# Optimization experiments

Hardware: AMD Instinct MI355X
Metric: run time of the kernel (lower is better)

The kernel has to match this reference:

```python
import jax, jax.numpy as jnp
import numpy as np

B, S, K = 4, 2048, 8
N_NEURONS, N_BASIS, RANK = 64, 32, 8
D_MODEL, D_HID = 256, 1024


def setup_inputs() -> dict:
    key = jax.random.key(0)
    ks = jax.random.split(key, 10)
    x = jax.random.normal(ks[0], (B, S, D_MODEL), dtype=jnp.float32)
    neuron_idx = jax.random.randint(ks[1], (B, S, K), 0, N_NEURONS)
    w = jax.random.uniform(ks[2], (B, S, K), dtype=jnp.float32)
    neuron_weights = w / jnp.sum(w, axis=-1, keepdims=True)  # softmax-like routing weights
    neuron_recipes = jax.random.normal(ks[3], (N_NEURONS, N_BASIS), dtype=jnp.float32) * 0.5
    sc = 0.1
    basis_A1 = jax.random.normal(ks[4], (N_BASIS, 16, RANK, 8), dtype=jnp.float32) * sc
    basis_A2 = jax.random.normal(ks[5], (N_BASIS, RANK, 16, 8), dtype=jnp.float32) * sc
    basis_B1 = jax.random.normal(ks[6], (N_BASIS, 8, RANK, 32), dtype=jnp.float32) * sc
    basis_B2 = jax.random.normal(ks[7], (N_BASIS, RANK, 8, 32), dtype=jnp.float32) * sc
    w_down_w = jax.random.normal(ks[8], (D_HID, D_MODEL), dtype=jnp.float32) * (1.0 / np.sqrt(D_HID))
    w_down_b = jnp.zeros((D_MODEL,), dtype=jnp.float32)
    return {
        "x": x, "neuron_idx": neuron_idx, "neuron_weights": neuron_weights,
        "neuron_recipes": neuron_recipes,
        "basis_A1": basis_A1, "basis_A2": basis_A2,
        "basis_B1": basis_B1, "basis_B2": basis_B2,
        "w_down_w": w_down_w, "w_down_b": w_down_b,
    }


def reference(x, neuron_idx, neuron_weights, neuron_recipes,
              basis_A1, basis_A2, basis_B1, basis_B2, w_down_w, w_down_b):
    Bt, St, D = x.shape
    # --- routing: gather recipes of selected neurons, softmax, weighted-combine ---
    sel = neuron_recipes[neuron_idx]                       # [B,S,k,n_basis]
    sel = jax.nn.softmax(sel, axis=-1)
    wr = jnp.einsum('bskn,bsk->bsn', sel, neuron_weights)  # [B,S,n_basis]
    # --- build per-token TT cores from basis banks (get_neuron_tt_cores) ---
    cA1 = jnp.einsum('bsn,nirk->bsirk', wr, basis_A1)      # [B,S,16,r,8]
    cA2 = jnp.einsum('bsn,nrjl->bsrjl', wr, basis_A2)      # [B,S,r,16,8]
    cB1 = jnp.einsum('bsn,nirk->bsirk', wr, basis_B1)      # [B,S,8,r,32]
    cB2 = jnp.einsum('bsn,nrjl->bsrjl', wr, basis_B2)      # [B,S,r,8,32]
    # --- TT FFN: 256 -> 64 ---
    x_fold = x.reshape(Bt, St, 16, 16)
    temp = jnp.einsum('bsij,bsirk->bsjrk', x_fold, cA1)
    h = jnp.einsum('bsjrk,bsrjl->bskl', temp, cA2).reshape(Bt, St, 64)
    # --- TT FFN: 64 -> 1024 ---
    h_fold = h.reshape(Bt, St, 8, 8)
    temp = jnp.einsum('bsij,bsirk->bsjrk', h_fold, cB1)
    out = jnp.einsum('bsjrk,bsrjl->bskl', temp, cB2).reshape(Bt, St, D_HID)
    out = jax.nn.gelu(out, approximate=False)              # torch F.gelu default = exact erf
    return out @ w_down_w + w_down_b                       # [B,S,256]
```

## Files before the change

kernel.cpp:

```cpp
#include <hip/hip_runtime.h>
#include <math.h>


typedef unsigned short u16;
typedef __attribute__((ext_vector_type(8))) __bf16 bf16x8;
typedef __attribute__((ext_vector_type(4))) float f32x4;
union ABCast { float4 f; bf16x8 v; };
union BFBits { __bf16 b; u16 u; };
union Pack8 { u16 u[8]; float4 f; };

__device__ __forceinline__ float gelu_exact(float v) {
    return 0.5f * v * (1.0f + erff(v * 0.70710678118654752440f));
}
__device__ __forceinline__ u16 f2bf_bits(float f) { BFBits c; c.b = (__bf16)f; return c.u; }
__device__ __forceinline__ float bfbits2f(u16 u) { BFBits c; c.u = u; return (float)c.b; }

__global__ __launch_bounds__(64) void k_route(
    const int* __restrict__ nidx, const float* __restrict__ nw,
    const float* __restrict__ recipes, float* __restrict__ wr_out,
    u16* __restrict__ wrAh, u16* __restrict__ wrAl)
{
    const int t = blockIdx.x * 64 + threadIdx.x;
    float acc[32];
#pragma unroll
    for (int n = 0; n < 32; n++) acc[n] = 0.f;
#pragma unroll
    for (int k = 0; k < 8; k++) {
        const int   id = nidx[t * 8 + k];
        const float wk = nw[t * 8 + k];
        const float4* row = (const float4*)(recipes + id * 32);
        float v[32];
#pragma unroll
        for (int q = 0; q < 8; q++) {
            float4 f = row[q];
            v[q*4+0] = f.x; v[q*4+1] = f.y; v[q*4+2] = f.z; v[q*4+3] = f.w;
        }
        float m = v[0];
#pragma unroll
        for (int n = 1; n < 32; n++) m = fmaxf(m, v[n]);
        float s = 0.f;
#pragma unroll
        for (int n = 0; n < 32; n++) { float e = expf(v[n] - m); v[n] = e; s += e; }
        const float iv = wk / s;
#pragma unroll
        for (int n = 0; n < 32; n++) acc[n] += v[n] * iv;
    }
    float4* o = (float4*)(wr_out + t * 32);
#pragma unroll
    for (int q = 0; q < 8; q++)
        o[q] = make_float4(acc[q*4+0], acc[q*4+1], acc[q*4+2], acc[q*4+3]);

    const int tg16 = t >> 4, tl = t & 15;
#pragma unroll
    for (int c = 0; c < 4; c++) {
        Pack8 ph, pl;
#pragma unroll
        for (int e = 0; e < 8; e++) {
            const float v = acc[c*8 + e];
            const u16 hb = f2bf_bits(v);
            ph.u[e] = hb;
            pl.u[e] = f2bf_bits(v - bfbits2f(hb));
        }
        const int lane = c * 16 + tl;
        *(float4*)(wrAh + (tg16*64 + lane)*8) = ph.f;
        *(float4*)(wrAl + (tg16*64 + lane)*8) = pl.f;
    }
}

__global__ __launch_bounds__(512) void k_stageA(
    const float* __restrict__ x, const float* __restrict__ wr,
    const float* __restrict__ A1, const float* __restrict__ A2,
    float* __restrict__ h_out)
{
    __shared__ float ca[8 * 1024];
    __shared__ float tl[8 * 1088];
    const int tid = threadIdx.x;
    const int t0  = blockIdx.x * 8;
    {
        const int e2 = tid * 2;
        float2 c[8];
#pragma unroll
        for (int tt = 0; tt < 8; tt++) c[tt] = make_float2(0.f, 0.f);
#pragma unroll 4
        for (int n = 0; n < 32; n++) {
            const float2 a = *(const float2*)(A1 + n * 1024 + e2);
#pragma unroll
            for (int tt = 0; tt < 8; tt++) {
                const float s = wr[(t0 + tt) * 32 + n];
                c[tt].x += s * a.x; c[tt].y += s * a.y;
            }
        }
#pragma unroll
        for (int tt = 0; tt < 8; tt++) *(float2*)(ca + tt * 1024 + e2) = c[tt];
    }
    __syncthreads();
    {
        const int t = tid >> 6, g = tid & 63, j = g >> 2, eh = g & 3;
        float xr[16];
#pragma unroll
        for (int i = 0; i < 16; i++) xr[i] = x[(t0 + t) * 256 + i * 16 + j];
        float tr[16];
#pragma unroll
        for (int q = 0; q < 16; q++) tr[q] = 0.f;
#pragma unroll
        for (int i = 0; i < 16; i++) {
            const float xv = xr[i];
#pragma unroll
            for (int q = 0; q < 4; q++) {
                const float4 cv = *(const float4*)(ca + t * 1024 + i * 64 + eh * 16 + q * 4);
                tr[q*4+0] += xv * cv.x; tr[q*4+1] += xv * cv.y;
                tr[q*4+2] += xv * cv.z; tr[q*4+3] += xv * cv.w;
            }
        }
#pragma unroll
        for (int q = 0; q < 4; q++)
            *(float4*)(tl + t * 1088 + j * 68 + eh * 16 + q * 4) =
                make_float4(tr[q*4+0], tr[q*4+1], tr[q*4+2], tr[q*4+3]);
    }
    __syncthreads();
    {
        const int e2 = tid * 2;
        float2 c[8];
#pragma unroll
        for (int tt = 0; tt < 8; tt++) c[tt] = make_float2(0.f, 0.f);
#pragma unroll 4
        for (int n = 0; n < 32; n++) {
            const float2 a = *(const float2*)(A2 + n * 1024 + e2);
#pragma unroll
            for (int tt = 0; tt < 8; tt++) {
                const float s = wr[(t0 + tt) * 32 + n];
                c[tt].x += s * a.x; c[tt].y += s * a.y;
            }
        }
#pragma unroll
        for (int tt = 0; tt < 8; tt++) *(float2*)(ca + tt * 1024 + e2) = c[tt];
    }
    __syncthreads();
    {
        const int t = tid >> 6, g = tid & 63, k = g >> 3, l = g & 7;
        float acc = 0.f;
#pragma unroll
        for (int j = 0; j < 16; j++) {
#pragma unroll
            for (int r = 0; r < 8; r++) {
                acc += tl[t * 1088 + j * 68 + r * 8 + k] *
                       ca[t * 1024 + r * 128 + j * 8 + l];
            }
        }
        h_out[(t0 + t) * 64 + g] = acc;
    }
}

__global__ __launch_bounds__(256) void k_bsplit(
    const float* __restrict__ B1, const float* __restrict__ B2,
    u16* __restrict__ o1h, u16* __restrict__ o1l,
    u16* __restrict__ o2h, u16* __restrict__ o2l)
{
    const int slot = blockIdx.x * 256 + threadIdx.x;
    const int bank = slot >> 13, r = (slot >> 10) & 7, g = (slot >> 6) & 15, l = slot & 63;
    const int c = l & 15, nb = 8 * (l >> 4);
    const int base = (bank == 0)
        ? ((g >> 1) * 256 + r * 32 + (g & 1) * 16 + c)
        : (r * 256 + (g >> 1) * 32 + (g & 1) * 16 + c);
    const float* S = (bank ? B2 : B1) + base + nb * 2048;
    Pack8 ph, pl;
#pragma unroll
    for (int e = 0; e < 8; e++) {
        const float v = S[e * 2048];
        const u16 hb = f2bf_bits(v);
        ph.u[e] = hb;
        pl.u[e] = f2bf_bits(v - bfbits2f(hb));
    }
    const int d = ((r * 16 + g) * 64 + l) * 8;
    *(float4*)((bank ? o2h : o1h) + d) = ph.f;
    *(float4*)((bank ? o2l : o1l) + d) = pl.f;
}

__global__ __launch_bounds__(256) void k_wsplit(
    const float* __restrict__ W, u16* __restrict__ wfh, u16* __restrict__ wfl)
{
    const int slot = blockIdx.x * 256 + threadIdx.x;
    const int ng = slot >> 11, kc = (slot >> 6) & 31, l = slot & 63;
    const float* S = W + (kc * 32 + 8 * (l >> 4)) * 256 + ng * 16 + (l & 15);
    Pack8 ph, pl;
#pragma unroll
    for (int e = 0; e < 8; e++) {
        const float v = S[e * 256];
        const u16 hb = f2bf_bits(v);
        ph.u[e] = hb;
        pl.u[e] = f2bf_bits(v - bfbits2f(hb));
    }
    const int d = ((ng * 32 + kc) * 64 + l) * 8;
    *(float4*)(wfh + d) = ph.f;
    *(float4*)(wfl + d) = pl.f;
}

__global__ __launch_bounds__(1024, 2) void k_fusedB(
    const float* __restrict__ hin,
    const u16* __restrict__ wrAh, const u16* __restrict__ wrAl,
    const u16* __restrict__ bf1h, const u16* __restrict__ bf1l,
    const u16* __restrict__ bf2h, const u16* __restrict__ bf2l,
    const u16* __restrict__ wfh, const u16* __restrict__ wfl,
    const float* __restrict__ bias, float* __restrict__ y)
{
    __shared__ __align__(16) unsigned char smem[65536];
    float* hs  = (float*)smem;
    float* cb1 = hs + 1024;
    float* cb2 = cb1 + 16 * 264;
    float* t2  = cb2 + 16 * 264;
    u16* gAh = (u16*)smem;
    u16* gAl = gAh + 16384;

    const int tid = threadIdx.x;
    const int l   = tid & 63;
    const int w   = tid >> 6;
    const int tg  = blockIdx.x;
    const int t0  = tg * 16;

    hs[tid] = hin[t0 * 64 + tid];

    ABCast cu;
    cu.f = *(const float4*)(wrAh + (tg * 64 + l) * 8); const bf16x8 wra_h = cu.v;
    cu.f = *(const float4*)(wrAl + (tg * 64 + l) * 8); const bf16x8 wra_l = cu.v;

    const bool isB2 = (w >= 8);
    const u16* bsrc_h = isB2 ? bf2h : bf1h;
    const u16* bsrc_l = isB2 ? bf2l : bf1l;
    float* cdst = isB2 ? cb2 : cb1;
    const int g0 = (w & 7) * 2;

    const int j2 = l >> 3, k42 = l & 7;
    const int k0 = (l & 7) * 4, l0 = (l >> 3) * 4;

    float o[4][4];
#pragma unroll
    for (int a = 0; a < 4; a++)
#pragma unroll
        for (int li = 0; li < 4; li++) o[a][li] = 0.f;

#pragma unroll 1
    for (int r = 0; r < 8; r++) {
#pragma unroll
        for (int gi = 0; gi < 2; gi++) {
            const int gg = g0 + gi;
            cu.f = *(const float4*)(bsrc_h + ((r*16 + gg)*64 + l)*8); const bf16x8 bh = cu.v;
            ABCast cu2;
            cu2.f = *(const float4*)(bsrc_l + ((r*16 + gg)*64 + l)*8); const bf16x8 bl = cu2.v;
            f32x4 cc = {0.f, 0.f, 0.f, 0.f};
            cc = __builtin_amdgcn_mfma_f32_16x16x32_bf16(wra_h, bh, cc, 0, 0, 0);
            cc = __builtin_amdgcn_mfma_f32_16x16x32_bf16(wra_h, bl, cc, 0, 0, 0);
            cc = __builtin_amdgcn_mfma_f32_16x16x32_bf16(wra_l, bh, cc, 0, 0, 0);
            float* cd = cdst + (gg >> 1) * 32 + (gg & 1) * 16 + (l & 15);
#pragma unroll
            for (int reg = 0; reg < 4; reg++)
                cd[(4 * (l >> 4) + reg) * 264] = cc[reg];
        }
        __syncthreads();

        {
            float4 acc = make_float4(0.f, 0.f, 0.f, 0.f);
#pragma unroll
            for (int i = 0; i < 8; i++) {
                const float  hv = hs[w * 64 + i * 8 + j2];
                const float4 cv = *(const float4*)(cb1 + w * 264 + i * 32 + k42 * 4);
                acc.x += hv * cv.x; acc.y += hv * cv.y;
                acc.z += hv * cv.z; acc.w += hv * cv.w;
            }
            *(float4*)(t2 + w * 264 + j2 * 32 + k42 * 4) = acc;
        }

        {
#pragma unroll
            for (int j = 0; j < 8; j++) {
                const float4 tv4 = *(const float4*)(t2  + w * 264 + j * 32 + k0);
                const float4 cv4 = *(const float4*)(cb2 + w * 264 + j * 32 + l0);
                const float tv[4] = {tv4.x, tv4.y, tv4.z, tv4.w};
                const float cv[4] = {cv4.x, cv4.y, cv4.z, cv4.w};
#pragma unroll
                for (int a = 0; a < 4; a++)
#pragma unroll
                    for (int li = 0; li < 4; li++)
                        o[a][li] += tv[a] * cv[li];
            }
        }
        __syncthreads();
    }

    {
        const int lane2 = (l0 >> 3) * 16 + w;
        const int e0 = l0 & 7;
#pragma unroll
        for (int a = 0; a < 4; a++) {
            u16 hv[4], lv[4];
#pragma unroll
            for (int li = 0; li < 4; li++) {
                const float v = gelu_exact(o[a][li]);
                const u16 hb = f2bf_bits(v);
                hv[li] = hb;
                lv[li] = f2bf_bits(v - bfbits2f(hb));
            }
            const int step = k0 + a;
            *(ushort4*)(gAh + (step * 64 + lane2) * 8 + e0) = make_ushort4(hv[0], hv[1], hv[2], hv[3]);
            *(ushort4*)(gAl + (step * 64 + lane2) * 8 + e0) = make_ushort4(lv[0], lv[1], lv[2], lv[3]);
        }
    }
    __syncthreads();

    f32x4 dacc = {0.f, 0.f, 0.f, 0.f};
    const int wb = w * 16384 + l * 8;
#pragma unroll 1
    for (int kc = 0; kc < 32; kc++) {
        cu.f = *(const float4*)(gAh + (kc * 64 + l) * 8); const bf16x8 ah = cu.v;
        cu.f = *(const float4*)(gAl + (kc * 64 + l) * 8); const bf16x8 al = cu.v;
        ABCast c0, c1;
        c0.f = *(const float4*)(wfh + wb + kc * 512); const bf16x8 bh = c0.v;
        c1.f = *(const float4*)(wfl + wb + kc * 512); const bf16x8 bl = c1.v;
        dacc = __builtin_amdgcn_mfma_f32_16x16x32_bf16(ah, bh, dacc, 0, 0, 0);
        dacc = __builtin_amdgcn_mfma_f32_16x16x32_bf16(ah, bl, dacc, 0, 0, 0);
        dacc = __builtin_amdgcn_mfma_f32_16x16x32_bf16(al, bh, dacc, 0, 0, 0);
    }
    {
        const int n0 = w * 16 + (l & 15);
        const float b0 = bias[n0];
        const int tb = t0 + 4 * (l >> 4);
#pragma unroll
        for (int reg = 0; reg < 4; reg++)
            y[(tb + reg) * 256 + n0] = dacc[reg] + b0;
    }
}

extern "C" void kernel_launch(void* const* d_in, const int* in_sizes, int n_in,
                              void* d_out, int out_size, void* d_ws, size_t ws_size,
                              hipStream_t stream)
{
    const float* x    = (const float*)d_in[0];
    const int*   nidx = (const int*)  d_in[1];
    const float* nw   = (const float*)d_in[2];
    const float* rec  = (const float*)d_in[3];
    const float* A1   = (const float*)d_in[4];
    const float* A2   = (const float*)d_in[5];
    const float* B1   = (const float*)d_in[6];
    const float* B2   = (const float*)d_in[7];
    const float* Wd   = (const float*)d_in[8];
    const float* bd   = (const float*)d_in[9];
    float* y  = (float*)d_out;

    float* wr  = (float*)d_ws;
    float* h   = wr + 8192 * 32;
    u16* wrAh  = (u16*)(h + 8192 * 64);
    u16* wrAl  = wrAh + 262144;
    u16* b1h   = wrAl + 262144;
    u16* b1l   = b1h + 65536;
    u16* b2h   = b1l + 65536;
    u16* b2l   = b2h + 65536;
    u16* wfh   = b2l + 65536;
    u16* wfl   = wfh + 262144;

    k_route <<<128,  64,   0, stream>>>(nidx, nw, rec, wr, wrAh, wrAl);
    k_stageA<<<1024, 512,  0, stream>>>(x, wr, A1, A2, h);
    k_bsplit<<<64,   256,  0, stream>>>(B1, B2, b1h, b1l, b2h, b2l);
    k_wsplit<<<128,  256,  0, stream>>>(Wd, wfh, wfl);
    k_fusedB<<<512,  1024, 0, stream>>>(h, wrAh, wrAl, b1h, b1l, b2h, b2l, wfh, wfl, bd, y);
}
```

Baseline: 104.6 us.

## Prefetch basis fragments, cache h in registers, halve waves in down-projection

The basis-bank fragments for the next rank step are loaded into registers ahead of time, so the global load overlaps the current step's MFMA and LDS work. The h values are read from shared memory once into registers and reused on every rank step. In the final down-projection only waves 0-7 run, each computing two 16-column output tiles so the A fragments from shared memory are shared between them. The risk is fewer active waves in the last phase and higher register pressure, which could lower latency hiding.

```diff
diff --git a/kernel.cpp b/kernel.cpp
--- a/kernel.cpp
+++ b/kernel.cpp
@@ -232,28 +232,56 @@
     const int j2 = l >> 3, k42 = l & 7;
     const int k0 = (l & 7) * 4, l0 = (l >> 3) * 4;
 
+    float hreg[8];
+#pragma unroll
+    for (int i = 0; i < 8; i++) hreg[i] = hs[w * 64 + i * 8 + j2];
+
     float o[4][4];
 #pragma unroll
     for (int a = 0; a < 4; a++)
 #pragma unroll
         for (int li = 0; li < 4; li++) o[a][li] = 0.f;
+
+    float4 pbh0 = *(const float4*)(bsrc_h + ((g0 + 0)*64 + l)*8);
+    float4 pbl0 = *(const float4*)(bsrc_l + ((g0 + 0)*64 + l)*8);
+    float4 pbh1 = *(const float4*)(bsrc_h + ((g0 + 1)*64 + l)*8);
+    float4 pbl1 = *(const float4*)(bsrc_l + ((g0 + 1)*64 + l)*8);
 
 #pragma unroll 1
     for (int r = 0; r < 8; r++) {
-#pragma unroll
-        for (int gi = 0; gi < 2; gi++) {
-            const int gg = g0 + gi;
-            cu.f = *(const float4*)(bsrc_h + ((r*16 + gg)*64 + l)*8); const bf16x8 bh = cu.v;
-            ABCast cu2;
-            cu2.f = *(const float4*)(bsrc_l + ((r*16 + gg)*64 + l)*8); const bf16x8 bl = cu2.v;
+        {
+            ABCast ch, cl2;
+            ch.f = pbh0; cl2.f = pbl0;
             f32x4 cc = {0.f, 0.f, 0.f, 0.f};
-            cc = __builtin_amdgcn_mfma_f32_16x16x32_bf16(wra_h, bh, cc, 0, 0, 0);
-            cc = __builtin_amdgcn_mfma_f32_16x16x32_bf16(wra_h, bl, cc, 0, 0, 0);
-            cc = __builtin_amdgcn_mfma_f32_16x16x32_bf16(wra_l, bh, cc, 0, 0, 0);
-            float* cd = cdst + (gg >> 1) * 32 + (gg & 1) * 16 + (l & 15);
-#pragma unroll
-            for (int reg = 0; reg < 4; reg++)
-                cd[(4 * (l >> 4) + reg) * 264] = cc[reg];
+            cc = __builtin_amdgcn_mfma_f32_16x16x32_bf16(wra_h, ch.v,  cc, 0, 0, 0);
+            cc = __builtin_amdgcn_mfma_f32_16x16x32_bf16(wra_h, cl2.v, cc, 0, 0, 0);
+            cc = __builtin_amdgcn_mfma_f32_16x16x32_bf16(wra_l, ch.v,  cc, 0, 0, 0);
+            {
+                const int gg = g0;
+                float* cd = cdst + (gg >> 1) * 32 + (gg & 1) * 16 + (l & 15);
+#pragma unroll
+                for (int reg = 0; reg < 4; reg++)
+                    cd[(4 * (l >> 4) + reg) * 264] = cc[reg];
+            }
+            ch.f = pbh1; cl2.f = pbl1;
+            f32x4 cc2 = {0.f, 0.f, 0.f, 0.f};
+            cc2 = __builtin_amdgcn_mfma_f32_16x16x32_bf16(wra_h, ch.v,  cc2, 0, 0, 0);
+            cc2 = __builtin_amdgcn_mfma_f32_16x16x32_bf16(wra_h, cl2.v, cc2, 0, 0, 0);
+            cc2 = __builtin_amdgcn_mfma_f32_16x16x32_bf16(wra_l, ch.v,  cc2, 0, 0, 0);
+            {
+                const int gg = g0 + 1;
+                float* cd = cdst + (gg >> 1) * 32 + (gg & 1) * 16 + (l & 15);
+#pragma unroll
+                for (int reg = 0; reg < 4; reg++)
+                    cd[(4 * (l >> 4) + reg) * 264] = cc2[reg];
+            }
+        }
+        if (r < 7) {
+            const int rb = (r + 1) * 16;
+            pbh0 = *(const float4*)(bsrc_h + ((rb + g0 + 0)*64 + l)*8);
+            pbl0 = *(const float4*)(bsrc_l + ((rb + g0 + 0)*64 + l)*8);
+            pbh1 = *(const float4*)(bsrc_h + ((rb + g0 + 1)*64 + l)*8);
+            pbl1 = *(const float4*)(bsrc_l + ((rb + g0 + 1)*64 + l)*8);
         }
         __syncthreads();
 
@@ -261,7 +289,7 @@
             float4 acc = make_float4(0.f, 0.f, 0.f, 0.f);
 #pragma unroll
             for (int i = 0; i < 8; i++) {
-                const float  hv = hs[w * 64 + i * 8 + j2];
+                const float  hv = hreg[i];
                 const float4 cv = *(const float4*)(cb1 + w * 264 + i * 32 + k42 * 4);
                 acc.x += hv * cv.x; acc.y += hv * cv.y;
                 acc.z += hv * cv.z; acc.w += hv * cv.w;
@@ -306,26 +334,35 @@
     }
     __syncthreads();
 
-    f32x4 dacc = {0.f, 0.f, 0.f, 0.f};
-    const int wb = w * 16384 + l * 8;
-#pragma unroll 1
-    for (int kc = 0; kc < 32; kc++) {
-        cu.f = *(const float4*)(gAh + (kc * 64 + l) * 8); const bf16x8 ah = cu.v;
-        cu.f = *(const float4*)(gAl + (kc * 64 + l) * 8); const bf16x8 al = cu.v;
-        ABCast c0, c1;
-        c0.f = *(const float4*)(wfh + wb + kc * 512); const bf16x8 bh = c0.v;
-        c1.f = *(const float4*)(wfl + wb + kc * 512); const bf16x8 bl = c1.v;
-        dacc = __builtin_amdgcn_mfma_f32_16x16x32_bf16(ah, bh, dacc, 0, 0, 0);
-        dacc = __builtin_amdgcn_mfma_f32_16x16x32_bf16(ah, bl, dacc, 0, 0, 0);
-        dacc = __builtin_amdgcn_mfma_f32_16x16x32_bf16(al, bh, dacc, 0, 0, 0);
-    }
-    {
+    if (w < 8) {
+        f32x4 dacc0 = {0.f, 0.f, 0.f, 0.f}, dacc1 = {0.f, 0.f, 0.f, 0.f};
+        const int wb0 = w * 16384 + l * 8;
+        const int wb1 = (w + 8) * 16384 + l * 8;
+#pragma unroll 2
+        for (int kc = 0; kc < 32; kc++) {
+            cu.f = *(const float4*)(gAh + (kc * 64 + l) * 8); const bf16x8 ah = cu.v;
+            cu.f = *(const float4*)(gAl + (kc * 64 + l) * 8); const bf16x8 al = cu.v;
+            ABCast c0, c1, c2, c3;
+            c0.f = *(const float4*)(wfh + wb0 + kc * 512); const bf16x8 bh0 = c0.v;
+            c1.f = *(const float4*)(wfl + wb0 + kc * 512); const bf16x8 bl0 = c1.v;
+            c2.f = *(const float4*)(wfh + wb1 + kc * 512); const bf16x8 bh1 = c2.v;
+            c3.f = *(const float4*)(wfl + wb1 + kc * 512); const bf16x8 bl1 = c3.v;
+            dacc0 = __builtin_amdgcn_mfma_f32_16x16x32_bf16(ah, bh0, dacc0, 0, 0, 0);
+            dacc0 = __builtin_amdgcn_mfma_f32_16x16x32_bf16(ah, bl0, dacc0, 0, 0, 0);
+            dacc0 = __builtin_amdgcn_mfma_f32_16x16x32_bf16(al, bh0, dacc0, 0, 0, 0);
+            dacc1 = __builtin_amdgcn_mfma_f32_16x16x32_bf16(ah, bh1, dacc1, 0, 0, 0);
+            dacc1 = __builtin_amdgcn_mfma_f32_16x16x32_bf16(ah, bl1, dacc1, 0, 0, 0);
+            dacc1 = __builtin_amdgcn_mfma_f32_16x16x32_bf16(al, bh1, dacc1, 0, 0, 0);
+        }
         const int n0 = w * 16 + (l & 15);
-        const float b0 = bias[n0];
+        const int n1 = (w + 8) * 16 + (l & 15);
+        const float b0 = bias[n0], b1 = bias[n1];
         const int tb = t0 + 4 * (l >> 4);
 #pragma unroll
-        for (int reg = 0; reg < 4; reg++)
-            y[(tb + reg) * 256 + n0] = dacc[reg] + b0;
+        for (int reg = 0; reg < 4; reg++) {
+            y[(tb + reg) * 256 + n0] = dacc0[reg] + b0;
+            y[(tb + reg) * 256 + n1] = dacc1[reg] + b1;
+        }
     }
 }
 
```

Result: faster. 101.1 us (-3.3%).
